# Kernel tuning notes

Hardware: AMD Instinct MI355X
Metric: run time of the kernel (lower is better)

## Reference

```python
import jax, jax.numpy as jnp
import numpy as np

N = 100000   # points in scan
K = 20       # KNN neighbors
D = 96       # backbone feature dim
H = 1024     # random-projection dim
C = 7        # num classes


def setup_inputs() -> dict:
    key = jax.random.key(0)
    ks = jax.random.split(key, 6)
    feat_source = jax.random.normal(ks[0], (N, D), jnp.float32)
    proto = jax.random.normal(ks[1], (C, D), jnp.float32)
    w_rand = jax.random.normal(ks[2], (D, H), jnp.float32)
    Q = jnp.zeros((H, C), jnp.float32)
    G = jnp.zeros((H, H), jnp.float32)
    coords = jax.random.normal(ks[3], (N, 3), jnp.float32) * 30.0
    normals_z = jax.random.uniform(ks[4], (N,), jnp.float32)
    near_indices = jax.random.randint(ks[5], (N, K), 0, N).astype(jnp.int64)
    return dict(feat_source=feat_source, proto=proto, w_rand=w_rand, Q=Q, G=G,
                coords=coords, normals_z=normals_z, near_indices=near_indices)


def _prior_filter(preds, coords, normals_z):
    plane_pred = (preds == 2) | (preds == 3) | (preds == 4)
    manmade_pred = preds == 5
    other = (preds == 0) | (preds == 1) | (preds == 6)
    ground = plane_pred & (normals_z > 0.9) & (coords[:, 2] < -10.0)
    g_index = ground | other | manmade_pred
    m_index = (manmade_pred & (normals_z < 0.1)) | other | plane_pred
    return g_index, m_index


def reference(feat_source, proto, w_rand, Q, G, coords, normals_z, near_indices):
    RIDGE = 100.0  # stand-in for optimise_ridge_parameter (source not provided)
    # prototype logits: feat @ normalize(proto, dim=1).T   [N, C]
    proto_n = proto / jnp.maximum(jnp.linalg.norm(proto, axis=1, keepdims=True), 1e-12)
    pred_proto = feat_source @ proto_n.T
    preds = jnp.argmax(pred_proto, axis=1)                       # [N]
    # KNN consistency filtering (irregular gather)
    neigh = preds[near_indices]                                  # [N, K]
    consistency = jnp.mean((neigh == preds[:, None]).astype(jnp.float32), axis=1)
    cmask = consistency > 0.8
    g_index, m_index = _prior_filter(preds, coords, normals_z)
    mask = cmask & g_index & m_index                             # [N]
    # random-projection features
    feat_h = jax.nn.relu(feat_source @ w_rand)                   # [N, H]
    yhat = jax.nn.one_hot(preds, C, dtype=feat_h.dtype)          # [N, C]
    mw = mask.astype(feat_h.dtype)[:, None]
    fh_m = feat_h * mw                                           # masked rows (mask^2 == mask)
    Qn = Q + jnp.einsum('nh,nc->hc', fh_m, yhat)
    Gn = G + fh_m.T @ fh_m
    # ridge solve: wo = solve(G + r*I, Q); module does feat_h @ wo
    wo = jnp.linalg.solve(Gn + RIDGE * jnp.eye(H, dtype=Gn.dtype), Qn)  # [H, C]
    pred_domain = feat_h @ wo                                    # [N, C]
    return pred_domain
```

## Files before the change

### kernel.cpp

```cpp
#include <hip/hip_runtime.h>

#define D_DIM 96
#define K_NN  20
#define H_DIM 1024
#define C_CLS 7


__global__ void k_preds(const float* __restrict__ feat,
                        const float* __restrict__ proto,
                        const long long* __restrict__ idx_ll,
                        int* __restrict__ preds, int* __restrict__ flags, int N) {
  __shared__ float4 pn4[C_CLS * (D_DIM / 4)];
  __shared__ float inv[C_CLS];
  __shared__ int any_big;
  const int t = threadIdx.x;
  if (t == 0) any_big = 0;
  if (t < C_CLS * (D_DIM / 4)) pn4[t] = ((const float4*)proto)[t];
  if (blockIdx.x == 0) {
    for (int j = t; j < 1024; j += blockDim.x) {
      long long v = idx_ll[j];
      if (v < 0 || v >= N) any_big = 1;
    }
  }
  __syncthreads();
  if (t < C_CLS) {
    const float* row = (const float*)&pn4[t * (D_DIM / 4)];
    float ss = 0.f;
    for (int d = 0; d < D_DIM; d++) ss += row[d] * row[d];
    inv[t] = 1.0f / fmaxf(sqrtf(ss), 1e-12f);
  }
  __syncthreads();
  if (t < C_CLS * (D_DIM / 4)) {
    float s = inv[t / (D_DIM / 4)];
    float4 v = pn4[t];
    v.x *= s; v.y *= s; v.z *= s; v.w *= s;
    pn4[t] = v;
  }
  if (blockIdx.x == 0 && t == 0) {
    flags[0] = 0;
    flags[1] = any_big ? 0 : 1;
  }
  __syncthreads();

  int i0 = blockIdx.x * 512 + t;
  int i1 = i0 + 256;
  int j0 = min(i0, N - 1), j1 = min(i1, N - 1);
  const float4* f0p = (const float4*)feat + (size_t)j0 * (D_DIM / 4);
  const float4* f1p = (const float4*)feat + (size_t)j1 * (D_DIM / 4);
  float s0[C_CLS], s1[C_CLS];
#pragma unroll
  for (int c = 0; c < C_CLS; c++) { s0[c] = 0.f; s1[c] = 0.f; }
#pragma unroll 4
  for (int q = 0; q < D_DIM / 4; q++) {
    float4 a = f0p[q];
    float4 b = f1p[q];
#pragma unroll
    for (int c = 0; c < C_CLS; c++) {
      float4 p = pn4[c * (D_DIM / 4) + q];
      s0[c] += a.x * p.x + a.y * p.y + a.z * p.z + a.w * p.w;
      s1[c] += b.x * p.x + b.y * p.y + b.z * p.z + b.w * p.w;
    }
  }
  float b0 = s0[0]; int a0 = 0;
  float b1 = s1[0]; int a1 = 0;
#pragma unroll
  for (int c = 1; c < C_CLS; c++) {
    if (s0[c] > b0) { b0 = s0[c]; a0 = c; }
    if (s1[c] > b1) { b1 = s1[c]; a1 = c; }
  }
  if (i0 < N) preds[i0] = a0;
  if (i1 < N) preds[i1] = a1;
}

__global__ void k_mask_copy(const int* __restrict__ preds, const void* __restrict__ nearv,
                            const float* __restrict__ coords, const float* __restrict__ normz,
                            int* __restrict__ flags, int* __restrict__ list,
                            const float* __restrict__ G, float* __restrict__ Gn, int N) {
  {
    const int total4 = (H_DIM * H_DIM) / 4;
    int stride = gridDim.x * blockDim.x;
    for (int v = blockIdx.x * blockDim.x + threadIdx.x; v < total4; v += stride)
      ((float4*)Gn)[v] = ((const float4*)G)[v];
  }
  int i = blockIdx.x * blockDim.x + threadIdx.x;
  if (i >= N) return;
  int p = preds[i];
  int idx[K_NN];
  if (flags[1]) {
    const longlong2* nn = (const longlong2*)((const long long*)nearv + (long long)i * K_NN);
#pragma unroll
    for (int k = 0; k < K_NN / 2; k++) {
      longlong2 v = nn[k];
      idx[2 * k] = (int)v.x; idx[2 * k + 1] = (int)v.y;
    }
  } else {
    const int4* nn = (const int4*)((const int*)nearv + (size_t)i * K_NN);
#pragma unroll
    for (int k = 0; k < K_NN / 4; k++) {
      int4 v = nn[k];
      idx[4 * k] = v.x; idx[4 * k + 1] = v.y; idx[4 * k + 2] = v.z; idx[4 * k + 3] = v.w;
    }
  }
  int cnt = 0;
#pragma unroll
  for (int k = 0; k < K_NN; k++) cnt += (preds[idx[k]] == p) ? 1 : 0;
  bool cmask = (cnt >= 17);
  bool plane = (p == 2) || (p == 3) || (p == 4);
  bool man   = (p == 5);
  bool other = (p == 0) || (p == 1) || (p == 6);
  float nz = normz[i];
  bool ground = plane && (nz > 0.9f) && (coords[(size_t)i * 3 + 2] < -10.0f);
  bool g = ground || other || man;
  bool m = (man && (nz < 0.1f)) || other || plane;
  if (cmask && g && m) {
    int pos = atomicAdd(&flags[0], 1);
    list[pos] = i;
  }
}

__device__ inline void block_reduce7(const float* val, volatile float* out,
                                     float* red) {
  int lane = threadIdx.x & 63, wave = threadIdx.x >> 6;
#pragma unroll
  for (int c = 0; c < C_CLS; c++) {
    float v = val[c];
#pragma unroll
    for (int o = 32; o > 0; o >>= 1) v += __shfl_down(v, o, 64);
    if (lane == 0) red[wave * C_CLS + c] = v;
  }
  __syncthreads();
  if (threadIdx.x == 0) {
#pragma unroll
    for (int c = 0; c < C_CLS; c++) {
      float s = 0.f;
      for (int wv = 0; wv < 16; wv++) s += red[wv * C_CLS + c];
      out[c] = s;
    }
  }
  __syncthreads();
}

__global__ void __launch_bounds__(1024) k_ridge(const float* __restrict__ feat,
                                                const float* __restrict__ w,
                                                const float* __restrict__ Q,
                                                const int* __restrict__ preds,
                                                const int* __restrict__ flags,
                                                const int* __restrict__ list,
                                                float* __restrict__ Gn,
                                                float* __restrict__ wo,
                                                float* __restrict__ wo_flag) {
  const int h = threadIdx.x;
  __shared__ float psh[H_DIM * C_CLS];
  __shared__ float red[16 * C_CLS];
  __shared__ float rs[C_CLS], bn2[C_CLS], pap[C_CLS], rsn[C_CLS];

  const int M = flags[0];
  float b[C_CLS];
#pragma unroll
  for (int c = 0; c < C_CLS; c++) b[c] = Q[h * C_CLS + c];
  for (int m = 0; m < M; m++) {
    int i = list[m];
    float s = 0.f;
    for (int d = 0; d < D_DIM; d++)
      s += feat[(size_t)i * D_DIM + d] * w[(size_t)d * H_DIM + h];
    s = fmaxf(s, 0.f);
    b[preds[i]] += s;
    psh[h] = s;
    __syncthreads();
    float sh = psh[h];
    for (int k = 0; k < H_DIM; k++)
      Gn[(size_t)h * H_DIM + k] += sh * psh[k];
    __syncthreads();
  }

  float x[C_CLS], r[C_CLS], p[C_CLS], t7[C_CLS];
#pragma unroll
  for (int c = 0; c < C_CLS; c++) {
    x[c] = 0.f; r[c] = b[c]; p[c] = b[c];
    t7[c] = b[c] * b[c];
  }
  block_reduce7(t7, rs, red);
  if (h == 0) {
#pragma unroll
    for (int c = 0; c < C_CLS; c++) bn2[c] = rs[c];
  }
  __syncthreads();

  for (int it = 0; it < H_DIM; it++) {
    bool done = true;
#pragma unroll
    for (int c = 0; c < C_CLS; c++)
      done = done && (rs[c] <= bn2[c] * 1e-16f + 1e-30f);
    if (done) break;

#pragma unroll
    for (int c = 0; c < C_CLS; c++) psh[h * C_CLS + c] = p[c];
    __syncthreads();

    float ap[C_CLS];
#pragma unroll
    for (int c = 0; c < C_CLS; c++) ap[c] = 100.0f * p[c];
    const float* grow = Gn + (size_t)h * H_DIM;
    for (int k = 0; k < H_DIM; k++) {
      float g = grow[k];
#pragma unroll
      for (int c = 0; c < C_CLS; c++) ap[c] += g * psh[k * C_CLS + c];
    }
#pragma unroll
    for (int c = 0; c < C_CLS; c++) t7[c] = p[c] * ap[c];
    block_reduce7(t7, pap, red);

    float a[C_CLS], rsold[C_CLS];
#pragma unroll
    for (int c = 0; c < C_CLS; c++) {
      rsold[c] = rs[c];
      bool act = rs[c] > bn2[c] * 1e-16f + 1e-30f;
      a[c] = act ? rsold[c] / fmaxf(pap[c], 1e-37f) : 0.f;
    }
#pragma unroll
    for (int c = 0; c < C_CLS; c++) {
      x[c] += a[c] * p[c];
      r[c] -= a[c] * ap[c];
      t7[c] = r[c] * r[c];
    }
    block_reduce7(t7, rsn, red);
#pragma unroll
    for (int c = 0; c < C_CLS; c++) {
      float bb = rsn[c] / fmaxf(rsold[c], 1e-37f);
      p[c] = r[c] + bb * p[c];
    }
    if (h == 0) {
#pragma unroll
      for (int c = 0; c < C_CLS; c++) rs[c] = rsn[c];
    }
    __syncthreads();
  }

#pragma unroll
  for (int c = 0; c < C_CLS; c++) wo[h * C_CLS + c] = x[c];
  float s = 0.f;
#pragma unroll
  for (int c = 0; c < C_CLS; c++) s += fabsf(x[c]);
  t7[0] = s;
#pragma unroll
  for (int c = 1; c < C_CLS; c++) t7[c] = 0.f;
  block_reduce7(t7, rsn, red);
  if (h == 0) *wo_flag = rsn[0];
}

__global__ void k_out(const float* __restrict__ feat, const float* __restrict__ w,
                      const float* __restrict__ wo, const float* __restrict__ wo_flag,
                      float* __restrict__ out, int N) {
  if (*wo_flag == 0.0f) {
    long long tid = (long long)blockIdx.x * blockDim.x + threadIdx.x;
    long long total = (long long)N * C_CLS;
    if (tid < total) out[tid] = 0.0f;
    return;
  }
  int i = blockIdx.x * blockDim.x + threadIdx.x;
  if (i >= N) return;
  float f[D_DIM];
  const float4* fp = (const float4*)(feat + (size_t)i * D_DIM);
#pragma unroll
  for (int q = 0; q < D_DIM / 4; q++) {
    float4 v = fp[q];
    f[4 * q] = v.x; f[4 * q + 1] = v.y; f[4 * q + 2] = v.z; f[4 * q + 3] = v.w;
  }
  float acc[C_CLS];
#pragma unroll
  for (int c = 0; c < C_CLS; c++) acc[c] = 0.f;
  for (int hh = 0; hh < H_DIM; hh++) {
    float s = 0.f;
#pragma unroll 8
    for (int d = 0; d < D_DIM; d++) s += f[d] * w[(size_t)d * H_DIM + hh];
    s = fmaxf(s, 0.f);
    const float* wrow = wo + hh * C_CLS;
#pragma unroll
    for (int c = 0; c < C_CLS; c++) acc[c] += s * wrow[c];
  }
#pragma unroll
  for (int c = 0; c < C_CLS; c++) out[(size_t)i * C_CLS + c] = acc[c];
}

extern "C" void kernel_launch(void* const* d_in, const int* in_sizes, int n_in,
                              void* d_out, int out_size, void* d_ws, size_t ws_size,
                              hipStream_t stream) {
  const float* feat   = (const float*)d_in[0];
  const float* proto  = (const float*)d_in[1];
  const float* w      = (const float*)d_in[2];
  const float* Q      = (const float*)d_in[3];
  const float* G      = (const float*)d_in[4];
  const float* coords = (const float*)d_in[5];
  const float* normz  = (const float*)d_in[6];
  const void*  nearv  = d_in[7];
  float* out = (float*)d_out;

  const int N = in_sizes[0] / D_DIM;

  char* WS = (char*)d_ws;
  int*   flags   = (int*)(WS + 4096);
  float* wo_flag = (float*)(WS + 4160);
  int*   preds   = (int*)(WS + 8192);
  int*   list    = (int*)(WS + 8192 + 400000);
  float* wo      = (float*)(WS + 836864);
  float* Gn      = (float*)(WS + 865536);
  if (ws_size < 5059840) return;

  int pblk = (N + 511) / 512;
  hipLaunchKernelGGL(k_preds, dim3(pblk), dim3(256), 0, stream,
                     feat, proto, (const long long*)nearv, preds, flags, N);
  int nblk = (N + 255) / 256;
  hipLaunchKernelGGL(k_mask_copy, dim3(nblk), dim3(256), 0, stream,
                     preds, nearv, coords, normz, flags, list, G, Gn, N);
  hipLaunchKernelGGL(k_ridge, dim3(1), dim3(1024), 0, stream,
                     feat, w, Q, preds, flags, list, Gn, wo, wo_flag);
  int oblk = (N * C_CLS + 255) / 256;
  hipLaunchKernelGGL(k_out, dim3(oblk), dim3(256), 0, stream,
                     feat, w, wo, wo_flag, out, N);
}
```

Baseline: 126.6 us.

## Skip G-to-Gn copy, read G directly when no masked rows; vectorize zero output

The mask kernel no longer copies the full 1024x1024 G matrix into the workspace. The ridge kernel now uses G directly as the system matrix when no rows pass the mask, and folds G into Gn on the first accumulated row otherwise. This removes a large read plus write of the matrix on every call. Separately, the prediction kernel handles one row per thread instead of two, and the all-zero output path writes float4 stores in a grid-stride loop with fewer blocks.

Measured after the change: 120.2 us. 5.1% less time.

```diff
diff --git a/kernel.cpp b/kernel.cpp
--- a/kernel.cpp
+++ b/kernel.cpp
@@ -42,46 +42,31 @@
   }
   __syncthreads();
 
-  int i0 = blockIdx.x * 512 + t;
-  int i1 = i0 + 256;
-  int j0 = min(i0, N - 1), j1 = min(i1, N - 1);
-  const float4* f0p = (const float4*)feat + (size_t)j0 * (D_DIM / 4);
-  const float4* f1p = (const float4*)feat + (size_t)j1 * (D_DIM / 4);
-  float s0[C_CLS], s1[C_CLS];
-#pragma unroll
-  for (int c = 0; c < C_CLS; c++) { s0[c] = 0.f; s1[c] = 0.f; }
+  int i = blockIdx.x * blockDim.x + t;
+  int j = min(i, N - 1);
+  const float4* fp = (const float4*)feat + (size_t)j * (D_DIM / 4);
+  float s[C_CLS];
+#pragma unroll
+  for (int c = 0; c < C_CLS; c++) s[c] = 0.f;
 #pragma unroll 4
   for (int q = 0; q < D_DIM / 4; q++) {
-    float4 a = f0p[q];
-    float4 b = f1p[q];
+    float4 a = fp[q];
 #pragma unroll
     for (int c = 0; c < C_CLS; c++) {
       float4 p = pn4[c * (D_DIM / 4) + q];
-      s0[c] += a.x * p.x + a.y * p.y + a.z * p.z + a.w * p.w;
-      s1[c] += b.x * p.x + b.y * p.y + b.z * p.z + b.w * p.w;
-    }
-  }
-  float b0 = s0[0]; int a0 = 0;
-  float b1 = s1[0]; int a1 = 0;
-#pragma unroll
-  for (int c = 1; c < C_CLS; c++) {
-    if (s0[c] > b0) { b0 = s0[c]; a0 = c; }
-    if (s1[c] > b1) { b1 = s1[c]; a1 = c; }
-  }
-  if (i0 < N) preds[i0] = a0;
-  if (i1 < N) preds[i1] = a1;
-}
-
-__global__ void k_mask_copy(const int* __restrict__ preds, const void* __restrict__ nearv,
-                            const float* __restrict__ coords, const float* __restrict__ normz,
-                            int* __restrict__ flags, int* __restrict__ list,
-                            const float* __restrict__ G, float* __restrict__ Gn, int N) {
-  {
-    const int total4 = (H_DIM * H_DIM) / 4;
-    int stride = gridDim.x * blockDim.x;
-    for (int v = blockIdx.x * blockDim.x + threadIdx.x; v < total4; v += stride)
-      ((float4*)Gn)[v] = ((const float4*)G)[v];
-  }
+      s[c] += a.x * p.x + a.y * p.y + a.z * p.z + a.w * p.w;
+    }
+  }
+  float best = s[0]; int bi = 0;
+#pragma unroll
+  for (int c = 1; c < C_CLS; c++)
+    if (s[c] > best) { best = s[c]; bi = c; }
+  if (i < N) preds[i] = bi;
+}
+
+__global__ void k_mask(const int* __restrict__ preds, const void* __restrict__ nearv,
+                       const float* __restrict__ coords, const float* __restrict__ normz,
+                       int* __restrict__ flags, int* __restrict__ list, int N) {
   int i = blockIdx.x * blockDim.x + threadIdx.x;
   if (i >= N) return;
   int p = preds[i];
@@ -143,6 +128,7 @@
 __global__ void __launch_bounds__(1024) k_ridge(const float* __restrict__ feat,
                                                 const float* __restrict__ w,
                                                 const float* __restrict__ Q,
+                                                const float* __restrict__ G,
                                                 const int* __restrict__ preds,
                                                 const int* __restrict__ flags,
                                                 const int* __restrict__ list,
@@ -158,19 +144,28 @@
   float b[C_CLS];
 #pragma unroll
   for (int c = 0; c < C_CLS; c++) b[c] = Q[h * C_CLS + c];
-  for (int m = 0; m < M; m++) {
-    int i = list[m];
-    float s = 0.f;
-    for (int d = 0; d < D_DIM; d++)
-      s += feat[(size_t)i * D_DIM + d] * w[(size_t)d * H_DIM + h];
-    s = fmaxf(s, 0.f);
-    b[preds[i]] += s;
-    psh[h] = s;
-    __syncthreads();
-    float sh = psh[h];
-    for (int k = 0; k < H_DIM; k++)
-      Gn[(size_t)h * H_DIM + k] += sh * psh[k];
-    __syncthreads();
+  const float* Amat = G;
+  if (M > 0) {
+    for (int m = 0; m < M; m++) {
+      int i = list[m];
+      float s = 0.f;
+      for (int d = 0; d < D_DIM; d++)
+        s += feat[(size_t)i * D_DIM + d] * w[(size_t)d * H_DIM + h];
+      s = fmaxf(s, 0.f);
+      b[preds[i]] += s;
+      psh[h] = s;
+      __syncthreads();
+      float sh = psh[h];
+      if (m == 0) {
+        for (int k = 0; k < H_DIM; k++)
+          Gn[(size_t)h * H_DIM + k] = G[(size_t)h * H_DIM + k] + sh * psh[k];
+      } else {
+        for (int k = 0; k < H_DIM; k++)
+          Gn[(size_t)h * H_DIM + k] += sh * psh[k];
+      }
+      __syncthreads();
+    }
+    Amat = Gn;
   }
 
   float x[C_CLS], r[C_CLS], p[C_CLS], t7[C_CLS];
@@ -200,7 +195,7 @@
     float ap[C_CLS];
 #pragma unroll
     for (int c = 0; c < C_CLS; c++) ap[c] = 100.0f * p[c];
-    const float* grow = Gn + (size_t)h * H_DIM;
+    const float* grow = Amat + (size_t)h * H_DIM;
     for (int k = 0; k < H_DIM; k++) {
       float g = grow[k];
 #pragma unroll
@@ -252,9 +247,11 @@
                       const float* __restrict__ wo, const float* __restrict__ wo_flag,
                       float* __restrict__ out, int N) {
   if (*wo_flag == 0.0f) {
-    long long tid = (long long)blockIdx.x * blockDim.x + threadIdx.x;
-    long long total = (long long)N * C_CLS;
-    if (tid < total) out[tid] = 0.0f;
+    int total4 = (N * C_CLS) / 4;
+    int stride = gridDim.x * blockDim.x;
+    float4 z = make_float4(0.f, 0.f, 0.f, 0.f);
+    for (int v = blockIdx.x * blockDim.x + threadIdx.x; v < total4; v += stride)
+      ((float4*)out)[v] = z;
     return;
   }
   int i = blockIdx.x * blockDim.x + threadIdx.x;
@@ -306,15 +303,14 @@
   float* Gn      = (float*)(WS + 865536);
   if (ws_size < 5059840) return;
 
-  int pblk = (N + 511) / 512;
-  hipLaunchKernelGGL(k_preds, dim3(pblk), dim3(256), 0, stream,
+  int nblk = (N + 255) / 256;
+  hipLaunchKernelGGL(k_preds, dim3(nblk), dim3(256), 0, stream,
                      feat, proto, (const long long*)nearv, preds, flags, N);
-  int nblk = (N + 255) / 256;
-  hipLaunchKernelGGL(k_mask_copy, dim3(nblk), dim3(256), 0, stream,
-                     preds, nearv, coords, normz, flags, list, G, Gn, N);
+  hipLaunchKernelGGL(k_mask, dim3(nblk), dim3(256), 0, stream,
+                     preds, nearv, coords, normz, flags, list, N);
   hipLaunchKernelGGL(k_ridge, dim3(1), dim3(1024), 0, stream,
-                     feat, w, Q, preds, flags, list, Gn, wo, wo_flag);
-  int oblk = (N * C_CLS + 255) / 256;
+                     feat, w, Q, G, preds, flags, list, Gn, wo, wo_flag);
+  int oblk = ((N * C_CLS) / 4 + 255) / 256;
   hipLaunchKernelGGL(k_out, dim3(oblk), dim3(256), 0, stream,
                      feat, w, wo, wo_flag, out, N);
 }
```
